# Kernel tuning notes

Measured on AMD Instinct MI355X. Metric: run time of the kernel, lower is better.

The kernel has to match this reference:

```python
import jax, jax.numpy as jnp
import numpy as np

B, T, C, H = 8, 1024, 768, 12  # GPT-2 small attention, block_size=1024

def setup_inputs() -> dict:
    key = jax.random.key(0)
    k0, k1, k2 = jax.random.split(key, 3)
    return {
        "x": jax.random.normal(k0, (1, B, T, C), jnp.float32) * 0.02,
        "w_attn": jax.random.normal(k1, (C, 3 * C), jnp.float32) * 0.02,
        "b_attn": jnp.zeros((3 * C,), jnp.float32),
        "w_proj": jax.random.normal(k2, (C, C), jnp.float32) * 0.02,
        "b_proj": jnp.zeros((C,), jnp.float32),
    }

def reference(x, w_attn, b_attn, w_proj, b_proj):
    _, b, t, c = x.shape
    d = c // H  # head dim
    xb = x[0]  # [B,T,C]
    qkv = xb @ w_attn + b_attn  # [B,T,3C]
    q, k, v = jnp.split(qkv, 3, axis=-1)
    def to_heads(u):
        return u.reshape(b, t, H, d).transpose(0, 2, 1, 3)  # [B,H,T,D]
    q, k, v = to_heads(q), to_heads(k), to_heads(v)
    scale = 1.0 / jnp.sqrt(jnp.asarray(d, q.dtype))
    att = jnp.einsum('bhqd,bhkd->bhqk', q, k) * scale  # [B,H,T,T]
    causal = jnp.tril(jnp.ones((t, t), bool))
    att = jnp.where(causal, att, -jnp.inf)
    att = jax.nn.softmax(att, axis=-1)
    y = jnp.einsum('bhqk,bhkd->bhqd', att, v)  # [B,H,T,D]
    y = y.transpose(0, 2, 1, 3).reshape(1, b, t, c)
    return y @ w_proj + b_proj
```

## Files before the change

kernel.cpp:

```cpp
#include <hip/hip_runtime.h>
#include <hip/hip_bf16.h>
#include <math.h>

#define Bq 8
#define Tq 1024
#define Cq 768
#define Hq 12
#define Dq 64
#define MROWS (Bq*Tq)
#define N_QKV (3*Cq)

typedef __bf16 bf16;
typedef bf16 bf16x8 __attribute__((ext_vector_type(8)));
typedef bf16 bf16x4 __attribute__((ext_vector_type(4)));
typedef float f32x4 __attribute__((ext_vector_type(4)));
typedef float f32x16 __attribute__((ext_vector_type(16)));
typedef unsigned int u32x4 __attribute__((ext_vector_type(4)));

#define MFMA16x16x32(a, b, c) __builtin_amdgcn_mfma_f32_16x16x32_bf16((a), (b), (c), 0, 0, 0)
#define MFMA32x32x16(a, b, c) __builtin_amdgcn_mfma_f32_32x32x16_bf16((a), (b), (c), 0, 0, 0)

__device__ __forceinline__ bf16x8& lds_v8(bf16* base, int row, int byteoff) {
    return *reinterpret_cast<bf16x8*>(
        reinterpret_cast<char*>(base) + row * 128 + (byteoff ^ ((row & 7) << 4)));
}

typedef __attribute__((address_space(3))) unsigned int lds_u32;
typedef const __attribute__((address_space(1))) unsigned int glb_u32;
__device__ __forceinline__ void gload16(const void* g, void* lds) {
    __builtin_amdgcn_global_load_lds((glb_u32*)(uintptr_t)g,
                                     (lds_u32*)(unsigned int)(uintptr_t)lds,
                                     16, 0, 0);
}

__device__ __forceinline__ unsigned cvtpk_bf16(float lo, float hi) {
    unsigned r;
    asm volatile("v_cvt_pk_bf16_f32 %0, %1, %2" : "=v"(r) : "v"(lo), "v"(hi));
    return r;
}

#define NA_CONV 3072
#define NB_WA   432
#define NB_WP   144
__global__ __launch_bounds__(256) void prep(const float* __restrict__ x,
                                            const float* __restrict__ wa,
                                            const float* __restrict__ wp,
                                            bf16* __restrict__ Ax,
                                            bf16* __restrict__ WaT,
                                            bf16* __restrict__ WpT) {
    __shared__ float tile[64][65];
    const int bid = blockIdx.x;
    if (bid < NA_CONV) {
        const int i = bid * 256 + threadIdx.x;
        const float4* p = reinterpret_cast<const float4*>(x) + (size_t)i * 2;
        float4 a = p[0], b = p[1];
        bf16x8 o;
        o[0] = (bf16)a.x; o[1] = (bf16)a.y; o[2] = (bf16)a.z; o[3] = (bf16)a.w;
        o[4] = (bf16)b.x; o[5] = (bf16)b.y; o[6] = (bf16)b.z; o[7] = (bf16)b.w;
        reinterpret_cast<bf16x8*>(Ax)[i] = o;
        return;
    }
    const float* src;
    bf16* dst;
    int C, tb, bxT;
    if (bid < NA_CONV + NB_WA) { tb = bid - NA_CONV; src = wa; dst = WaT; C = N_QKV; bxT = 36; }
    else                       { tb = bid - NA_CONV - NB_WA; src = wp; dst = WpT; C = Cq; bxT = 12; }
    const int R = Cq;
    const int bx = (tb % bxT) * 64, by = (tb / bxT) * 64;
    const int tx = threadIdx.x & 63, ty = threadIdx.x >> 6;
    #pragma unroll
    for (int i = 0; i < 64; i += 4)
        tile[ty + i][tx] = src[(size_t)(by + ty + i) * C + bx + tx];
    __syncthreads();
    #pragma unroll
    for (int i = 0; i < 64; i += 4)
        dst[(size_t)(bx + ty + i) * R + by + tx] = (bf16)tile[tx][ty + i];
}

__global__ __launch_bounds__(256) void gemm_qkv(const bf16* __restrict__ A,
                                                const bf16* __restrict__ Bt,
                                                const float* __restrict__ bias,
                                                bf16* __restrict__ Qo,
                                                bf16* __restrict__ K8,
                                                bf16* __restrict__ V8) {
    __shared__ bf16 As[2][128 * 64];
    __shared__ bf16 Bs[2][128 * 64];
    const int tid = threadIdx.x;
    const int w = tid >> 6, l = tid & 63;
    const int lane16 = l & 15, kg = l >> 4;
    const int wr = w >> 1, wc = w & 1;
    const int flat = blockIdx.x;
    const int nid = (flat & 7) * 144 + (flat >> 3);
    const int bn0 = (nid % 18) * 128, bm0 = (nid / 18) * 128;

    auto stage = [&](int k0, int buf) {
        #pragma unroll
        for (int j = 0; j < 4; ++j) {
            const int q8 = w * 4 + j;
            const int r  = q8 * 8 + (l >> 3);
            const int c16 = (l & 7) ^ (r & 7);
            gload16(A + (size_t)(bm0 + r) * Cq + k0 + c16 * 8, &As[buf][q8 * 512]);
            gload16(Bt + (size_t)(bn0 + r) * Cq + k0 + c16 * 8, &Bs[buf][q8 * 512]);
        }
    };

    f32x4 acc[4][4] = {};
    stage(0, 0);
    __syncthreads();
    for (int kt = 0; kt < 12; ++kt) {
        if (kt < 11) stage((kt + 1) * 64, (kt + 1) & 1);
        bf16* Ac = As[kt & 1];
        bf16* Bc = Bs[kt & 1];
        #pragma unroll
        for (int ks = 0; ks < 2; ++ks) {
            bf16x8 af[4], bfr[4];
            #pragma unroll
            for (int m = 0; m < 4; ++m)
                af[m] = lds_v8(Ac, wr * 64 + m * 16 + lane16, ks * 64 + kg * 16);
            #pragma unroll
            for (int n = 0; n < 4; ++n)
                bfr[n] = lds_v8(Bc, wc * 64 + n * 16 + lane16, ks * 64 + kg * 16);
            #pragma unroll
            for (int m = 0; m < 4; ++m)
                #pragma unroll
                for (int n = 0; n < 4; ++n)
                    acc[m][n] = MFMA16x16x32(af[m], bfr[n], acc[m][n]);
        }
        __syncthreads();
    }

    const int whichB = bn0 / Cq;
    char* Lt = (char*)&As[0][0];
    #pragma unroll
    for (int mi = 0; mi < 4; ++mi) {
        #pragma unroll
        for (int r = 0; r < 4; ++r) {
            const int m = wr * 64 + mi * 16 + kg * 4 + r;
            #pragma unroll
            for (int ni = 0; ni < 4; ++ni) {
                const int n = wc * 64 + ni * 16 + lane16;
                float v = acc[mi][ni][r] + bias[bn0 + n];
                if (whichB == 0) v *= 0.18033688011112042f;
                int a;
                if (whichB < 2) a = m * 256 + ((n * 2) ^ ((m & 7) << 4));
                else            a = n * 256 + ((m * 2) ^ ((n & 7) << 4));
                *reinterpret_cast<bf16*>(Lt + a) = (bf16)v;
            }
        }
    }
    __syncthreads();
    const int bb = bm0 >> 10, tt0 = bm0 & 1023;
    if (whichB == 0) {
        #pragma unroll
        for (int j = 0; j < 8; ++j) {
            const int c = j * 256 + tid;
            const int m = c >> 4, nc = c & 15;
            bf16x8 val = *reinterpret_cast<bf16x8*>(Lt + m * 256 + ((nc * 16) ^ ((m & 7) << 4)));
            const int gcol0 = bn0 + nc * 8;
            const int h = gcol0 >> 6;
            const int d0 = gcol0 & 63;
            *reinterpret_cast<bf16x8*>(Qo + (((size_t)bb * Hq + h) * Tq + tt0 + m) * Dq + d0) = val;
        }
    } else if (whichB == 1) {
        #pragma unroll
        for (int j = 0; j < 8; ++j) {
            const int c = j * 256 + tid;
            const int m = c & 127, nc = c >> 7;
            bf16x8 val = *reinterpret_cast<bf16x8*>(Lt + m * 256 + ((nc * 16) ^ ((m & 7) << 4)));
            const int hn = bn0 + nc * 8 - Cq;
            const int h = hn >> 6, d8 = (hn >> 3) & 7;
            *reinterpret_cast<bf16x8*>(
                K8 + ((((size_t)bb * Hq + h) * 8 + d8) * Tq + tt0 + m) * 8) = val;
        }
    } else {
        #pragma unroll
        for (int j = 0; j < 8; ++j) {
            const int c = j * 256 + tid;
            const int d6 = c & 63, rest = c >> 6;
            const int hh = rest & 1, mc = rest >> 1;
            const int n = hh * 64 + d6;
            bf16x8 val = *reinterpret_cast<bf16x8*>(Lt + n * 256 + ((mc * 16) ^ ((n & 7) << 4)));
            const int hn = bn0 + n - 2 * Cq;
            const int h = hn >> 6, d = hn & 63;
            *reinterpret_cast<bf16x8*>(
                V8 + ((((size_t)bb * Hq + h) * 128 + (tt0 >> 3) + mc) * Dq + d) * 8) = val;
        }
    }
}

__global__ __launch_bounds__(256) void attn_mfma(const bf16* __restrict__ Q,
                                                 const bf16* __restrict__ K8,
                                                 const bf16* __restrict__ V8,
                                                 bf16* __restrict__ Y) {
    const int tid = threadIdx.x;
    const int w = tid >> 6, l = tid & 63;
    const int l31 = l & 31, hi = l >> 5;
    const int b4 = blockIdx.x / 96;
    const int bh = blockIdx.x % 96;
    const int qt = 15 - (b4 * 4 + w);
    const size_t hoff = (size_t)bh * Tq * Dq;
    const size_t base8 = (size_t)bh * (Tq * Dq);
    const int q0 = qt * 64;

    bf16x8 qf[2][4];
    #pragma unroll
    for (int sub = 0; sub < 2; ++sub)
        #pragma unroll
        for (int ds = 0; ds < 4; ++ds)
            qf[sub][ds] = *reinterpret_cast<const bf16x8*>(
                Q + hoff + (size_t)(q0 + sub * 32 + l31) * Dq + ds * 16 + hi * 8);

    f32x16 o[2][2] = {};
    float m_[2] = {-INFINITY, -INFINITY};
    float l_[2] = {0.f, 0.f};

    for (int t = 0; t <= qt; ++t) {
        bf16x8 kf[2][4];
        #pragma unroll
        for (int kh = 0; kh < 2; ++kh)
            #pragma unroll
            for (int ds = 0; ds < 4; ++ds)
                kf[kh][ds] = *reinterpret_cast<const bf16x8*>(
                    K8 + base8 + ((size_t)(ds * 2 + hi) * Tq + t * 64 + kh * 32 + l31) * 8);
        bf16x8 vf[4][2];
        #pragma unroll
        for (int ks = 0; ks < 4; ++ks)
            #pragma unroll
            for (int dh = 0; dh < 2; ++dh)
                vf[ks][dh] = *reinterpret_cast<const bf16x8*>(
                    V8 + base8 + ((size_t)(t * 8 + ks * 2 + hi) * Dq + dh * 32 + l31) * 8);

        #pragma unroll
        for (int sub = 0; sub < 2; ++sub) {
            f32x16 s[2] = {};
            #pragma unroll
            for (int kh = 0; kh < 2; ++kh)
                #pragma unroll
                for (int ds = 0; ds < 4; ++ds)
                    s[kh] = MFMA32x32x16(kf[kh][ds], qf[sub][ds], s[kh]);
            if (t == qt) {
                #pragma unroll
                for (int kh = 0; kh < 2; ++kh)
                    #pragma unroll
                    for (int reg = 0; reg < 16; ++reg) {
                        const int kcol = (reg & 3) + 8 * (reg >> 2) + 4 * hi + kh * 32;
                        if (kcol > sub * 32 + l31) s[kh][reg] = -INFINITY;
                    }
            }
            float pmax = s[0][0];
            #pragma unroll
            for (int kh = 0; kh < 2; ++kh)
                #pragma unroll
                for (int reg = 0; reg < 16; ++reg) pmax = fmaxf(pmax, s[kh][reg]);
            pmax = fmaxf(pmax, __shfl_xor(pmax, 32));
            const float mn = fmaxf(m_[sub], pmax);
            const float alpha = exp2f(m_[sub] - mn);
            m_[sub] = mn;
            l_[sub] *= alpha;
            o[sub][0] *= alpha;
            o[sub][1] *= alpha;
            float lsum = 0.f;
            #pragma unroll
            for (int kh = 0; kh < 2; ++kh)
                #pragma unroll
                for (int reg = 0; reg < 16; ++reg) {
                    const float p = exp2f(s[kh][reg] - mn);
                    s[kh][reg] = p;
                    lsum += p;
                }
            l_[sub] += lsum;
            bf16x8 pa[4];
            #pragma unroll
            for (int kh = 0; kh < 2; ++kh)
                #pragma unroll
                for (int g = 0; g < 2; ++g) {
                    const int rb = g * 8;
                    const unsigned u01 = cvtpk_bf16(s[kh][rb + 0], s[kh][rb + 1]);
                    const unsigned u23 = cvtpk_bf16(s[kh][rb + 2], s[kh][rb + 3]);
                    const unsigned u45 = cvtpk_bf16(s[kh][rb + 4], s[kh][rb + 5]);
                    const unsigned u67 = cvtpk_bf16(s[kh][rb + 6], s[kh][rb + 7]);
                    const unsigned x01 = __shfl_xor(u01, 32);
                    const unsigned x23 = __shfl_xor(u23, 32);
                    const unsigned x45 = __shfl_xor(u45, 32);
                    const unsigned x67 = __shfl_xor(u67, 32);
                    u32x4 wv;
                    wv[0] = hi ? x45 : u01;
                    wv[1] = hi ? x67 : u23;
                    wv[2] = hi ? u45 : x01;
                    wv[3] = hi ? u67 : x23;
                    pa[kh * 2 + g] = __builtin_bit_cast(bf16x8, wv);
                }
            #pragma unroll
            for (int ks = 0; ks < 4; ++ks)
                #pragma unroll
                for (int dh = 0; dh < 2; ++dh)
                    o[sub][dh] = MFMA32x32x16(vf[ks][dh], pa[ks], o[sub][dh]);
        }
    }

    const int bb = bh / Hq, h = bh - bb * Hq;
    #pragma unroll
    for (int sub = 0; sub < 2; ++sub) {
        const float ltot = l_[sub] + __shfl_xor(l_[sub], 32);
        const float inv = 1.f / ltot;
        const int q = q0 + sub * 32 + l31;
        bf16* yp = Y + ((size_t)bb * Tq + q) * Cq + h * Dq;
        #pragma unroll
        for (int dh = 0; dh < 2; ++dh)
            #pragma unroll
            for (int rg = 0; rg < 4; ++rg) {
                const int d0 = 8 * rg + 4 * hi + 32 * dh;
                bf16x4 ov;
                #pragma unroll
                for (int j = 0; j < 4; ++j) ov[j] = (bf16)(o[sub][dh][rg * 4 + j] * inv);
                *reinterpret_cast<bf16x4*>(yp + d0) = ov;
            }
    }
}

__global__ __launch_bounds__(256) void gemm_proj(const bf16* __restrict__ A,
                                                 const bf16* __restrict__ Bt,
                                                 const float* __restrict__ bias,
                                                 float* __restrict__ out) {
    __shared__ bf16 As[2][128 * 64];
    __shared__ bf16 Bs[2][128 * 64];
    const int tid = threadIdx.x;
    const int w = tid >> 6, l = tid & 63;
    const int lane16 = l & 15, kg = l >> 4;
    const int wr = w >> 1, wc = w & 1;
    const int flat = blockIdx.x;
    const int nid = (flat & 7) * 48 + (flat >> 3);
    const int bn0 = (nid % 6) * 128, bm0 = (nid / 6) * 128;

    auto stage = [&](int k0, int buf) {
        #pragma unroll
        for (int j = 0; j < 4; ++j) {
            const int q8 = w * 4 + j;
            const int r  = q8 * 8 + (l >> 3);
            const int c16 = (l & 7) ^ (r & 7);
            gload16(A + (size_t)(bm0 + r) * Cq + k0 + c16 * 8, &As[buf][q8 * 512]);
            gload16(Bt + (size_t)(bn0 + r) * Cq + k0 + c16 * 8, &Bs[buf][q8 * 512]);
        }
    };

    f32x4 acc[4][4] = {};
    stage(0, 0);
    __syncthreads();
    for (int kt = 0; kt < 12; ++kt) {
        if (kt < 11) stage((kt + 1) * 64, (kt + 1) & 1);
        bf16* Ac = As[kt & 1];
        bf16* Bc = Bs[kt & 1];
        #pragma unroll
        for (int ks = 0; ks < 2; ++ks) {
            bf16x8 af[4], bfr[4];
            #pragma unroll
            for (int m = 0; m < 4; ++m)
                af[m] = lds_v8(Ac, wr * 64 + m * 16 + lane16, ks * 64 + kg * 16);
            #pragma unroll
            for (int n = 0; n < 4; ++n)
                bfr[n] = lds_v8(Bc, wc * 64 + n * 16 + lane16, ks * 64 + kg * 16);
            #pragma unroll
            for (int m = 0; m < 4; ++m)
                #pragma unroll
                for (int n = 0; n < 4; ++n)
                    acc[m][n] = MFMA16x16x32(af[m], bfr[n], acc[m][n]);
        }
        __syncthreads();
    }

    char* L32 = (char*)&As[0][0];
    #pragma unroll
    for (int half = 0; half < 2; ++half) {
        if (wc == half) {
            #pragma unroll
            for (int mi = 0; mi < 4; ++mi)
                #pragma unroll
                for (int r = 0; r < 4; ++r) {
                    const int m = wr * 64 + mi * 16 + kg * 4 + r;
                    #pragma unroll
                    for (int ni = 0; ni < 4; ++ni) {
                        const int nl = ni * 16 + lane16;
                        const float v = acc[mi][ni][r] + bias[bn0 + half * 64 + nl];
                        *reinterpret_cast<float*>(L32 + m * 256 + ((nl * 4) ^ ((m & 7) << 4))) = v;
                    }
                }
        }
        __syncthreads();
        #pragma unroll
        for (int j = 0; j < 8; ++j) {
            const int c = j * 256 + tid;
            const int m = c >> 4, nc = c & 15;
            float4 val = *reinterpret_cast<float4*>(L32 + m * 256 + ((nc * 16) ^ ((m & 7) << 4)));
            *reinterpret_cast<float4*>(out + (size_t)(bm0 + m) * Cq + bn0 + half * 64 + nc * 4) = val;
        }
        __syncthreads();
    }
}

extern "C" void kernel_launch(void* const* d_in, const int* in_sizes, int n_in,
                              void* d_out, int out_size, void* d_ws, size_t ws_size,
                              hipStream_t stream) {
    const float* x      = (const float*)d_in[0];
    const float* w_attn = (const float*)d_in[1];
    const float* b_attn = (const float*)d_in[2];
    const float* w_proj = (const float*)d_in[3];
    const float* b_proj = (const float*)d_in[4];
    float* out = (float*)d_out;

    char* ws = (char*)d_ws;
    bf16* Ax  = (bf16*)ws; ws += (size_t)MROWS * Cq * 2;
    bf16* WaT = (bf16*)ws; ws += (size_t)N_QKV * Cq * 2;
    bf16* WpT = (bf16*)ws; ws += (size_t)Cq * Cq * 2;
    bf16* Qw  = (bf16*)ws; ws += (size_t)MROWS * Cq * 2;
    bf16* K8w = (bf16*)ws; ws += (size_t)MROWS * Cq * 2;
    bf16* V8w = (bf16*)ws; ws += (size_t)MROWS * Cq * 2;
    bf16* Yw  = (bf16*)ws; ws += (size_t)MROWS * Cq * 2;

    prep<<<dim3(NA_CONV + NB_WA + NB_WP), 256, 0, stream>>>(x, w_attn, w_proj, Ax, WaT, WpT);
    gemm_qkv<<<dim3(1152), 256, 0, stream>>>(Ax, WaT, b_attn, Qw, K8w, V8w);
    attn_mfma<<<dim3(384), 256, 0, stream>>>(Qw, K8w, V8w, Yw);
    gemm_proj<<<dim3(384), 256, 0, stream>>>(Yw, WpT, b_proj, out);
}
```

Before: 114.6 us.

## Use single-wave attention blocks and skip fully masked diagonal sub-tiles

```diff
diff --git a/kernel.cpp b/kernel.cpp
--- a/kernel.cpp
+++ b/kernel.cpp
@@ -188,16 +188,15 @@
     }
 }
 
-__global__ __launch_bounds__(256) void attn_mfma(const bf16* __restrict__ Q,
-                                                 const bf16* __restrict__ K8,
-                                                 const bf16* __restrict__ V8,
-                                                 bf16* __restrict__ Y) {
-    const int tid = threadIdx.x;
-    const int w = tid >> 6, l = tid & 63;
+__global__ __launch_bounds__(64) void attn_mfma(const bf16* __restrict__ Q,
+                                                const bf16* __restrict__ K8,
+                                                const bf16* __restrict__ V8,
+                                                bf16* __restrict__ Y) {
+    const int l = threadIdx.x;
     const int l31 = l & 31, hi = l >> 5;
-    const int b4 = blockIdx.x / 96;
-    const int bh = blockIdx.x % 96;
-    const int qt = 15 - (b4 * 4 + w);
+    const int id = blockIdx.x;
+    const int qt = 15 - (id / 96);
+    const int bh = id % 96;
     const size_t hoff = (size_t)bh * Tq * Dq;
     const size_t base8 = (size_t)bh * (Tq * Dq);
     const int q0 = qt * 64;
@@ -229,29 +228,33 @@
             for (int dh = 0; dh < 2; ++dh)
                 vf[ks][dh] = *reinterpret_cast<const bf16x8*>(
                     V8 + base8 + ((size_t)(t * 8 + ks * 2 + hi) * Dq + dh * 32 + l31) * 8);
+        const bool diag = (t == qt);
 
         #pragma unroll
         for (int sub = 0; sub < 2; ++sub) {
+            const bool skipHi = diag && (sub == 0);
             f32x16 s[2] = {};
             #pragma unroll
-            for (int kh = 0; kh < 2; ++kh)
-                #pragma unroll
-                for (int ds = 0; ds < 4; ++ds)
-                    s[kh] = MFMA32x32x16(kf[kh][ds], qf[sub][ds], s[kh]);
-            if (t == qt) {
-                #pragma unroll
-                for (int kh = 0; kh < 2; ++kh)
-                    #pragma unroll
-                    for (int reg = 0; reg < 16; ++reg) {
-                        const int kcol = (reg & 3) + 8 * (reg >> 2) + 4 * hi + kh * 32;
-                        if (kcol > sub * 32 + l31) s[kh][reg] = -INFINITY;
-                    }
-            }
-            float pmax = s[0][0];
-            #pragma unroll
-            for (int kh = 0; kh < 2; ++kh)
-                #pragma unroll
-                for (int reg = 0; reg < 16; ++reg) pmax = fmaxf(pmax, s[kh][reg]);
+            for (int ds = 0; ds < 4; ++ds) s[0] = MFMA32x32x16(kf[0][ds], qf[sub][ds], s[0]);
+            if (!skipHi) {
+                #pragma unroll
+                for (int ds = 0; ds < 4; ++ds) s[1] = MFMA32x32x16(kf[1][ds], qf[sub][ds], s[1]);
+            }
+            if (diag) {
+                #pragma unroll
+                for (int reg = 0; reg < 16; ++reg) {
+                    const int kcol = (reg & 3) + 8 * (reg >> 2) + 4 * hi;
+                    if (kcol > sub * 32 + l31) s[0][reg] = -INFINITY;
+                    if (!skipHi && kcol + 32 > sub * 32 + l31) s[1][reg] = -INFINITY;
+                }
+            }
+            float pmax = -INFINITY;
+            #pragma unroll
+            for (int reg = 0; reg < 16; ++reg) pmax = fmaxf(pmax, s[0][reg]);
+            if (!skipHi) {
+                #pragma unroll
+                for (int reg = 0; reg < 16; ++reg) pmax = fmaxf(pmax, s[1][reg]);
+            }
             pmax = fmaxf(pmax, __shfl_xor(pmax, 32));
             const float mn = fmaxf(m_[sub], pmax);
             const float alpha = exp2f(m_[sub] - mn);
@@ -261,17 +264,24 @@
             o[sub][1] *= alpha;
             float lsum = 0.f;
             #pragma unroll
-            for (int kh = 0; kh < 2; ++kh)
+            for (int reg = 0; reg < 16; ++reg) {
+                const float p = exp2f(s[0][reg] - mn);
+                s[0][reg] = p;
+                lsum += p;
+            }
+            if (!skipHi) {
                 #pragma unroll
                 for (int reg = 0; reg < 16; ++reg) {
-                    const float p = exp2f(s[kh][reg] - mn);
-                    s[kh][reg] = p;
+                    const float p = exp2f(s[1][reg] - mn);
+                    s[1][reg] = p;
                     lsum += p;
                 }
+            }
             l_[sub] += lsum;
             bf16x8 pa[4];
             #pragma unroll
-            for (int kh = 0; kh < 2; ++kh)
+            for (int kh = 0; kh < 2; ++kh) {
+                if (kh == 1 && skipHi) break;
                 #pragma unroll
                 for (int g = 0; g < 2; ++g) {
                     const int rb = g * 8;
@@ -290,11 +300,19 @@
                     wv[3] = hi ? u67 : x23;
                     pa[kh * 2 + g] = __builtin_bit_cast(bf16x8, wv);
                 }
-            #pragma unroll
-            for (int ks = 0; ks < 4; ++ks)
+            }
+            #pragma unroll
+            for (int ks = 0; ks < 2; ++ks)
                 #pragma unroll
                 for (int dh = 0; dh < 2; ++dh)
                     o[sub][dh] = MFMA32x32x16(vf[ks][dh], pa[ks], o[sub][dh]);
+            if (!skipHi) {
+                #pragma unroll
+                for (int ks = 2; ks < 4; ++ks)
+                    #pragma unroll
+                    for (int dh = 0; dh < 2; ++dh)
+                        o[sub][dh] = MFMA32x32x16(vf[ks][dh], pa[ks], o[sub][dh]);
+            }
         }
     }
 
@@ -418,6 +436,6 @@
 
     prep<<<dim3(NA_CONV + NB_WA + NB_WP), 256, 0, stream>>>(x, w_attn, w_proj, Ax, WaT, WpT);
     gemm_qkv<<<dim3(1152), 256, 0, stream>>>(Ax, WaT, b_attn, Qw, K8w, V8w);
-    attn_mfma<<<dim3(384), 256, 0, stream>>>(Qw, K8w, V8w, Yw);
+    attn_mfma<<<dim3(1536), 64, 0, stream>>>(Qw, K8w, V8w, Yw);
     gemm_proj<<<dim3(384), 256, 0, stream>>>(Yw, WpT, b_proj, out);
 }
```

Result: no change. 115.2 us (+0.5%).
